# Kernel optimization log

Hardware: AMD Instinct MI355X
Metric: run time of the kernel (lower is better)

Reference implementation:

```python
import jax, jax.numpy as jnp
import numpy as np

AMPLITUDE_STD = 4.2  # repo constant (unexported); normalization scale for ln_mag
EPS = 1e-8


def _interp_bias(table, x):
    # Linear interpolation of a 1D table over frequency domain [-1, 1].
    n = table.shape[0]
    idx = jnp.clip((x + 1.0) * 0.5 * (n - 1), 0.0, float(n - 1))
    i0 = jnp.floor(idx).astype(jnp.int32)
    i1 = jnp.minimum(i0 + 1, n - 1)
    w = idx - i0.astype(idx.dtype)
    return table[i0] * (1.0 - w) + table[i1] * w


def setup_inputs() -> dict:
    key = jax.random.key(0)
    k1, k2, k3, k4 = jax.random.split(key, 4)
    B, F, P, W, H = 8, 128, 32, 96, 96
    return {
        "mode_shapes": jax.random.normal(k1, (B, 2, P, W, H), dtype=jnp.float32),
        "mode_responses": jax.random.normal(k2, (B, F, 2, P), dtype=jnp.float32),
        "freqs": jax.random.uniform(k3, (B, F), dtype=jnp.float32, minval=-1.0, maxval=1.0),
        "bias_table": jax.random.normal(k4, (250,), dtype=jnp.float32) * 0.1,
    }


def reference(mode_shapes, mode_responses, freqs, bias_table):
    B, _, P, W, H = mode_shapes.shape
    F = mode_responses.shape[1]
    # _normalize_mode: L2 norm over (real/imag, W, H) per (batch, peak)
    norm = jnp.sqrt(jnp.sum(mode_shapes ** 2, axis=(1, 3, 4)))  # (B,P)
    ms = mode_shapes / (norm[:, None, :, None, None] + EPS)
    s_r, s_i = ms[:, 0], ms[:, 1]                                # (B,P,W,H)
    t_r, t_i = mode_responses[:, :, 0], mode_responses[:, :, 1]  # (B,F,P)
    f = 1.0 / P
    # complex superposition over modes: contraction over n_peaks
    rr = jnp.einsum('bpwh,bfp->bfwh', s_r, t_r)
    ii = jnp.einsum('bpwh,bfp->bfwh', s_i, t_i)
    ri = jnp.einsum('bpwh,bfp->bfwh', s_r, t_i)
    ir = jnp.einsum('bpwh,bfp->bfwh', s_i, t_r)
    r_new = f * (rr - ii)  # (B,F,W,H)
    i_new = f * (ri + ir)
    mag2 = r_new ** 2 + i_new ** 2
    bias = _interp_bias(bias_table, freqs)                       # (B,F)
    ln_mag = (jnp.log(mag2 + EPS) + bias[:, :, None, None]) / AMPLITUDE_STD
    fnorm = jnp.sum(mag2, axis=(-1, -2), keepdims=True)
    fnorm = jnp.sqrt(jnp.clip(fnorm, jnp.finfo(fnorm.dtype).eps))
    normed_field = jnp.stack([r_new / fnorm, i_new / fnorm], axis=2)  # (B,F,2,W,H)
    # aux sparsity loss over mode responses
    mr = mode_responses.reshape(B, F * 2, P)
    aux_sparse = jnp.mean(jnp.mean(jnp.log(jnp.linalg.norm(mr, axis=1) + 1.0), axis=1))
    return ln_mag, normed_field, aux_sparse
```

## Files before the change

### kernel.cpp

```cpp
#include <hip/hip_runtime.h>
#include <math.h>

#define WHN 9216
#define PN 32
#define FN 128
#define BN 8
#define EPSF 1e-8f
#define INV_STD 0.23809523809f
#define AUX_IDX 28311552

typedef __attribute__((ext_vector_type(8))) short short8;
typedef __attribute__((ext_vector_type(16))) float f32x16;

__device__ __forceinline__ unsigned short f2bf(float x) {
  unsigned int u = __float_as_uint(x);
  unsigned int r = (u + 0x7FFFu + ((u >> 16) & 1u)) >> 16;
  return (unsigned short)r;
}
__device__ __forceinline__ float bf2f(unsigned short h) {
  return __uint_as_float(((unsigned int)h) << 16);
}

__global__ __launch_bounds__(256) void k_gram(const float* __restrict__ ms,
                                              float* __restrict__ wsM,
                                              float* __restrict__ wsA,
                                              float* __restrict__ part,
                                              int use_part) {
  const int b = blockIdx.y;
  const int chunk = blockIdx.x;
  const int tid = threadIdx.x;
  __shared__ float4 sA[32][32];
  __shared__ float4 sB[32][32];
  __shared__ float pbuf[2][2048];
  const float4* ms4 = (const float4*)ms;
#pragma unroll
  for (int k = 0; k < 4; ++k) {
    int i4 = tid + k * 256;
    int xq = i4 & 31, p = i4 >> 5;
    sA[xq][p ^ xq] = ms4[((b * 2 + 0) * 32 + p) * 2304 + chunk * 32 + xq];
    sB[xq][p ^ xq] = ms4[((b * 2 + 1) * 32 + p) * 2304 + chunk * 32 + xq];
  }
  __syncthreads();
  const int w = tid >> 6, lane = tid & 63;
  const int pg = lane & 7, qg = lane >> 3;
  float accM[4][4] = {{0}}, accA[4][4] = {{0}};
  for (int xq = w; xq < 32; xq += 4) {
    float4 pa[4], pb[4], qa[4], qb[4];
#pragma unroll
    for (int j = 0; j < 4; ++j) {
      pa[j] = sA[xq][(pg + 8 * j) ^ xq];
      pb[j] = sB[xq][(pg + 8 * j) ^ xq];
      qa[j] = sA[xq][(qg + 8 * j) ^ xq];
      qb[j] = sB[xq][(qg + 8 * j) ^ xq];
    }
#pragma unroll
    for (int j = 0; j < 4; ++j)
#pragma unroll
      for (int k = 0; k < 4; ++k) {
        accM[j][k] += pa[j].x * qa[k].x + pb[j].x * qb[k].x
                    + pa[j].y * qa[k].y + pb[j].y * qb[k].y
                    + pa[j].z * qa[k].z + pb[j].z * qb[k].z
                    + pa[j].w * qa[k].w + pb[j].w * qb[k].w;
        accA[j][k] += pa[j].x * qb[k].x - pb[j].x * qa[k].x
                    + pa[j].y * qb[k].y - pb[j].y * qa[k].y
                    + pa[j].z * qb[k].z - pb[j].z * qa[k].z
                    + pa[j].w * qb[k].w - pb[j].w * qa[k].w;
      }
  }
  if (w < 2) {
#pragma unroll
    for (int j = 0; j < 4; ++j)
#pragma unroll
      for (int k = 0; k < 4; ++k) {
        pbuf[w][lane * 32 + j * 4 + k] = accM[j][k];
        pbuf[w][lane * 32 + 16 + j * 4 + k] = accA[j][k];
      }
  }
  __syncthreads();
  if (w >= 2) {
#pragma unroll
    for (int j = 0; j < 4; ++j)
#pragma unroll
      for (int k = 0; k < 4; ++k) {
        pbuf[w - 2][lane * 32 + j * 4 + k] += accM[j][k];
        pbuf[w - 2][lane * 32 + 16 + j * 4 + k] += accA[j][k];
      }
  }
  __syncthreads();
  for (int idx = tid; idx < 2048; idx += 256) {
    float v = pbuf[0][idx] + pbuf[1][idx];
    if (use_part) {
      part[((size_t)(b * 72 + chunk)) * 2048 + idx] = v;
    } else {
      int lane2 = idx >> 5, r = idx & 31;
      int mat = r >> 4, rr = r & 15, j = rr >> 2, k = rr & 3;
      int p = (lane2 & 7) + 8 * j, q = (lane2 >> 3) + 8 * k;
      float* dst = mat ? wsA : wsM;
      atomicAdd(dst + (b << 10) + p * 32 + q, v);
    }
  }
}

__global__ __launch_bounds__(256) void k_reduce(const float* __restrict__ part,
                                                float* __restrict__ wsM,
                                                float* __restrict__ wsA,
                                                float* __restrict__ wsc) {
  int g = blockIdx.x * 256 + threadIdx.x;
  int b = g >> 11, idx = g & 2047;
  const float* p = part + ((size_t)b * 72) * 2048 + idx;
  float s = 0.f;
#pragma unroll 8
  for (int c = 0; c < 72; ++c) s += p[(size_t)c * 2048];
  int lane2 = idx >> 5, r = idx & 31;
  int mat = r >> 4, rr = r & 15, j = rr >> 2, k = rr & 3;
  int pp = (lane2 & 7) + 8 * j, q = (lane2 >> 3) + 8 * k;
  (mat ? wsA : wsM)[(b << 10) + pp * 32 + q] = s;
  if (!mat && pp == q) wsc[(b << 5) + pp] = (1.0f / 32.0f) / (sqrtf(s) + EPSF);
}

__global__ void k_cfromM(const float* __restrict__ wsM, float* __restrict__ wsc) {
  int tid = threadIdx.x;
  int b = tid >> 5, p = tid & 31;
  float m = wsM[(b << 10) + p * 33];
  wsc[tid] = (1.0f / 32.0f) / (sqrtf(m) + EPSF);
}

__global__ __launch_bounds__(256) void k_aux(const float* __restrict__ t,
                                             float* __restrict__ out) {
  const int b = blockIdx.x, tid = threadIdx.x;
  const float4* t4 = (const float4*)t + (size_t)b * 2048;
  float4 a; a.x = a.y = a.z = a.w = 0.f;
#pragma unroll
  for (int j = 0; j < 8; ++j) {
    float4 v = t4[tid + j * 256];
    a.x = fmaf(v.x, v.x, a.x);
    a.y = fmaf(v.y, v.y, a.y);
    a.z = fmaf(v.z, v.z, a.z);
    a.w = fmaf(v.w, v.w, a.w);
  }
#pragma unroll
  for (int off = 8; off <= 32; off <<= 1) {
    a.x += __shfl_xor(a.x, off);
    a.y += __shfl_xor(a.y, off);
    a.z += __shfl_xor(a.z, off);
    a.w += __shfl_xor(a.w, off);
  }
  __shared__ float sred[4][8][4];
  int wv = tid >> 6, lane = tid & 63;
  if (lane < 8) {
    sred[wv][lane][0] = a.x; sred[wv][lane][1] = a.y;
    sred[wv][lane][2] = a.z; sred[wv][lane][3] = a.w;
  }
  __syncthreads();
  if (tid < 8) {
    float s0 = 0, s1 = 0, s2 = 0, s3 = 0;
#pragma unroll
    for (int w2 = 0; w2 < 4; ++w2) {
      s0 += sred[w2][tid][0]; s1 += sred[w2][tid][1];
      s2 += sred[w2][tid][2]; s3 += sred[w2][tid][3];
    }
    float val = logf(sqrtf(s0) + 1.f) + logf(sqrtf(s1) + 1.f)
              + logf(sqrtf(s2) + 1.f) + logf(sqrtf(s3) + 1.f);
    val += __shfl_xor(val, 1);
    val += __shfl_xor(val, 2);
    val += __shfl_xor(val, 4);
    if (tid == 0) atomicAdd(out + AUX_IDX, val * (1.0f / 256.0f));
  }
}

__global__ __launch_bounds__(64) void k_fnorm(const float* __restrict__ t,
                                              const float* __restrict__ freqs,
                                              const float* __restrict__ btab,
                                              const float* __restrict__ wsM,
                                              const float* __restrict__ wsA,
                                              const float* __restrict__ wsc,
                                              float* __restrict__ wsinv,
                                              float* __restrict__ wsbias) {
  const int bf = blockIdx.x;
  const int b = bf >> 7;
  const int lane = threadIdx.x;
  __shared__ float tt[64];
  {
    int p = lane & 31, comp = lane >> 5;
    tt[lane] = t[(bf * 2 + comp) * PN + p] * wsc[(b << 5) + p];
  }
  __syncthreads();
  const int pp = lane & 31, qh = lane >> 5;
  const float* Mrow = wsM + (b << 10) + pp * 32 + qh * 16;
  const float* Arow = wsA + (b << 10) + pp * 32 + qh * 16;
  float ap = tt[pp], bp = tt[32 + pp];
  float S = 0.f;
#pragma unroll
  for (int k = 0; k < 16; ++k) {
    int q = qh * 16 + k;
    float aq = tt[q], bq = tt[32 + q];
    S += (ap * aq + bp * bq) * Mrow[k] + 2.0f * (bp * aq) * Arow[k];
  }
#pragma unroll
  for (int off = 32; off; off >>= 1) S += __shfl_xor(S, off);
  if (lane == 0) {
    float fn = sqrtf(fmaxf(S, 1.1920929e-7f));
    wsinv[bf] = 1.0f / fn;
    float x = freqs[bf];
    float idx = (x + 1.0f) * 0.5f * 249.0f;
    idx = fminf(fmaxf(idx, 0.0f), 249.0f);
    float fi = floorf(idx);
    int i0 = (int)fi;
    int i1 = min(i0 + 1, 249);
    float wvv = idx - fi;
    wsbias[bf] = btab[i0] * (1.0f - wvv) + btab[i1] * wvv;
  }
}

#define MFMA32(A, B, C) __builtin_amdgcn_mfma_f32_32x32x16_bf16(A, B, C, 0, 0, 0)
__global__ __launch_bounds__(256) void k_main(const float* __restrict__ ms,
                                              const float* __restrict__ t,
                                              const float* __restrict__ wsc,
                                              const float* __restrict__ wsinv,
                                              const float* __restrict__ wsbias,
                                              float* __restrict__ out) {
  __shared__ short tHs[8192];
  __shared__ short tLs[8192];
  __shared__ float sInv[128], sBias[128], sC[32];
  const int b = blockIdx.y;
  const int tid = threadIdx.x;
  const int lane = tid & 63, wv = tid >> 6;
  const int col = lane & 31, hf = lane >> 5;
  const int pix = blockIdx.x * 128 + wv * 32 + col;

  short8 sHf[4], sLf[4];
#pragma unroll
  for (int kg = 0; kg < 4; ++kg) {
#pragma unroll
    for (int j = 0; j < 8; ++j) {
      int k = kg * 16 + hf * 8 + j;
      float v = ms[(((size_t)b * 2 + (k >> 5)) * 32 + (k & 31)) * WHN + pix];
      unsigned short h = f2bf(v);
      sHf[kg][j] = (short)h;
      sLf[kg][j] = (short)f2bf(v - bf2f(h));
    }
  }
  short8 msk;
#pragma unroll
  for (int j = 0; j < 8; ++j) msk[j] = (short)0x8000;
  short8 nH2 = sHf[2] ^ msk, nL2 = sLf[2] ^ msk;
  short8 nH3 = sHf[3] ^ msk, nL3 = sLf[3] ^ msk;

  if (tid < 128) sInv[tid] = wsinv[b * 128 + tid];
  else sBias[tid - 128] = wsbias[b * 128 + (tid - 128)];
  if (tid < 32) sC[tid] = wsc[b * 32 + tid];
  __syncthreads();

#pragma unroll
  for (int it = 0; it < 4; ++it) {
    int gidx = tid + it * 256;
    int f = gidx >> 3, g = gidx & 7;
    const float* src = t + ((size_t)(b * 128 + f) * 2 + (g >> 2)) * 32 + (g & 3) * 8;
    int gs = g ^ (f & 7);
    short8 hv, lv;
#pragma unroll
    for (int e = 0; e < 8; ++e) {
      float v = src[e] * sC[(g & 3) * 8 + e];
      unsigned short h = f2bf(v);
      hv[e] = (short)h;
      lv[e] = (short)f2bf(v - bf2f(h));
    }
    *(short8*)&tHs[f * 64 + gs * 8] = hv;
    *(short8*)&tLs[f * 64 + gs * 8] = lv;
  }
  __syncthreads();

  float* outF = out + (size_t)BN * FN * WHN;

  for (int ft = 0; ft < 4; ++ft) {
    short8 tHf[4], tLf[4];
    int f = ft * 32 + col;
    int fx = f & 7;
#pragma unroll
    for (int kg = 0; kg < 4; ++kg) {
      int gs = (2 * kg + hf) ^ fx;
      tHf[kg] = *(const short8*)&tHs[f * 64 + gs * 8];
      tLf[kg] = *(const short8*)&tLs[f * 64 + gs * 8];
    }
    f32x16 aR, aI;
#pragma unroll
    for (int i = 0; i < 16; ++i) { aR[i] = 0.f; aI[i] = 0.f; }
    aR = MFMA32(tHf[0], sHf[0], aR); aR = MFMA32(tHf[0], sLf[0], aR); aR = MFMA32(tLf[0], sHf[0], aR);
    aR = MFMA32(tHf[1], sHf[1], aR); aR = MFMA32(tHf[1], sLf[1], aR); aR = MFMA32(tLf[1], sHf[1], aR);
    aR = MFMA32(tHf[2], nH2,    aR); aR = MFMA32(tHf[2], nL2,    aR); aR = MFMA32(tLf[2], nH2,    aR);
    aR = MFMA32(tHf[3], nH3,    aR); aR = MFMA32(tHf[3], nL3,    aR); aR = MFMA32(tLf[3], nH3,    aR);
    aI = MFMA32(tHf[0], sHf[2], aI); aI = MFMA32(tHf[0], sLf[2], aI); aI = MFMA32(tLf[0], sHf[2], aI);
    aI = MFMA32(tHf[1], sHf[3], aI); aI = MFMA32(tHf[1], sLf[3], aI); aI = MFMA32(tLf[1], sHf[3], aI);
    aI = MFMA32(tHf[2], sHf[0], aI); aI = MFMA32(tHf[2], sLf[0], aI); aI = MFMA32(tLf[2], sHf[0], aI);
    aI = MFMA32(tHf[3], sHf[1], aI); aI = MFMA32(tHf[3], sLf[1], aI); aI = MFMA32(tLf[3], sHf[1], aI);
#pragma unroll
    for (int r = 0; r < 16; ++r) {
      int row = (r & 3) + 8 * (r >> 2) + 4 * hf;
      int fo = ft * 32 + row;
      float vr = aR[r], vi = aI[r];
      float mag2 = fmaf(vr, vr, vi * vi);
      float ln = (__logf(mag2 + EPSF) + sBias[fo]) * INV_STD;
      float inv = sInv[fo];
      size_t fg = (size_t)(b * 128 + fo);
      out[fg * WHN + pix] = ln;
      outF[(fg * 2) * WHN + pix] = vr * inv;
      outF[(fg * 2 + 1) * WHN + pix] = vi * inv;
    }
  }
}

extern "C" void kernel_launch(void* const* d_in, const int* in_sizes, int n_in,
                              void* d_out, int out_size, void* d_ws, size_t ws_size,
                              hipStream_t stream) {
  const float* ms = (const float*)d_in[0];
  const float* t  = (const float*)d_in[1];
  const float* fr = (const float*)d_in[2];
  const float* bt = (const float*)d_in[3];
  float* out = (float*)d_out;
  float* ws = (float*)d_ws;
  float* wsM = ws;
  float* wsA = ws + 8192;
  float* wsc = ws + 16384;
  float* wsinv = ws + 16640;
  float* wsbias = ws + 17664;
  float* part = ws + 18688;
  size_t need = ((size_t)18688 + (size_t)576 * 2048) * 4;
  int use_part = (ws_size >= need) ? 1 : 0;

  hipMemsetAsync((char*)d_out + (size_t)AUX_IDX * 4, 0, 4, stream);
  if (use_part) {
    hipLaunchKernelGGL(k_gram, dim3(72, 8), dim3(256), 0, stream, ms, wsM, wsA, part, 1);
    hipLaunchKernelGGL(k_reduce, dim3(64), dim3(256), 0, stream, part, wsM, wsA, wsc);
  } else {
    hipMemsetAsync(ws, 0, 16384 * sizeof(float), stream);
    hipLaunchKernelGGL(k_gram, dim3(72, 8), dim3(256), 0, stream, ms, wsM, wsA, part, 0);
    hipLaunchKernelGGL(k_cfromM, dim3(1), dim3(256), 0, stream, wsM, wsc);
  }
  hipLaunchKernelGGL(k_fnorm, dim3(1024), dim3(64), 0, stream, t, fr, bt, wsM, wsA, wsc, wsinv, wsbias);
  hipLaunchKernelGGL(k_aux, dim3(8), dim3(256), 0, stream, t, out);
  hipLaunchKernelGGL(k_main, dim3(72, 8), dim3(256), 0, stream, ms, t, wsc, wsinv, wsbias, out);
}
```

Measured before the change: 168.9 us.

## Split main kernel over frequency halves, fold aux into fnorm, drop memset

```diff
diff --git a/kernel.cpp b/kernel.cpp
--- a/kernel.cpp
+++ b/kernel.cpp
@@ -101,11 +101,13 @@
   }
 }
 
-__global__ __launch_bounds__(256) void k_reduce(const float* __restrict__ part,
-                                                float* __restrict__ wsM,
-                                                float* __restrict__ wsA,
-                                                float* __restrict__ wsc) {
+__global__ __launch_bounds__(256) void k_mid(const float* __restrict__ part,
+                                             float* __restrict__ wsM,
+                                             float* __restrict__ wsA,
+                                             float* __restrict__ wsc,
+                                             float* __restrict__ out) {
   int g = blockIdx.x * 256 + threadIdx.x;
+  if (g == 0) out[AUX_IDX] = 0.f;
   int b = g >> 11, idx = g & 2047;
   const float* p = part + ((size_t)b * 72) * 2048 + idx;
   float s = 0.f;
@@ -118,67 +120,43 @@
   if (!mat && pp == q) wsc[(b << 5) + pp] = (1.0f / 32.0f) / (sqrtf(s) + EPSF);
 }
 
-__global__ void k_cfromM(const float* __restrict__ wsM, float* __restrict__ wsc) {
+__global__ void k_cfromM(const float* __restrict__ wsM, float* __restrict__ wsc,
+                         float* __restrict__ out) {
   int tid = threadIdx.x;
+  if (tid == 0) out[AUX_IDX] = 0.f;
   int b = tid >> 5, p = tid & 31;
   float m = wsM[(b << 10) + p * 33];
   wsc[tid] = (1.0f / 32.0f) / (sqrtf(m) + EPSF);
 }
 
-__global__ __launch_bounds__(256) void k_aux(const float* __restrict__ t,
-                                             float* __restrict__ out) {
-  const int b = blockIdx.x, tid = threadIdx.x;
-  const float4* t4 = (const float4*)t + (size_t)b * 2048;
-  float4 a; a.x = a.y = a.z = a.w = 0.f;
-#pragma unroll
-  for (int j = 0; j < 8; ++j) {
-    float4 v = t4[tid + j * 256];
-    a.x = fmaf(v.x, v.x, a.x);
-    a.y = fmaf(v.y, v.y, a.y);
-    a.z = fmaf(v.z, v.z, a.z);
-    a.w = fmaf(v.w, v.w, a.w);
-  }
-#pragma unroll
-  for (int off = 8; off <= 32; off <<= 1) {
-    a.x += __shfl_xor(a.x, off);
-    a.y += __shfl_xor(a.y, off);
-    a.z += __shfl_xor(a.z, off);
-    a.w += __shfl_xor(a.w, off);
-  }
-  __shared__ float sred[4][8][4];
-  int wv = tid >> 6, lane = tid & 63;
-  if (lane < 8) {
-    sred[wv][lane][0] = a.x; sred[wv][lane][1] = a.y;
-    sred[wv][lane][2] = a.z; sred[wv][lane][3] = a.w;
-  }
-  __syncthreads();
-  if (tid < 8) {
-    float s0 = 0, s1 = 0, s2 = 0, s3 = 0;
-#pragma unroll
-    for (int w2 = 0; w2 < 4; ++w2) {
-      s0 += sred[w2][tid][0]; s1 += sred[w2][tid][1];
-      s2 += sred[w2][tid][2]; s3 += sred[w2][tid][3];
-    }
-    float val = logf(sqrtf(s0) + 1.f) + logf(sqrtf(s1) + 1.f)
-              + logf(sqrtf(s2) + 1.f) + logf(sqrtf(s3) + 1.f);
-    val += __shfl_xor(val, 1);
-    val += __shfl_xor(val, 2);
-    val += __shfl_xor(val, 4);
-    if (tid == 0) atomicAdd(out + AUX_IDX, val * (1.0f / 256.0f));
-  }
-}
-
-__global__ __launch_bounds__(64) void k_fnorm(const float* __restrict__ t,
-                                              const float* __restrict__ freqs,
-                                              const float* __restrict__ btab,
-                                              const float* __restrict__ wsM,
-                                              const float* __restrict__ wsA,
-                                              const float* __restrict__ wsc,
-                                              float* __restrict__ wsinv,
-                                              float* __restrict__ wsbias) {
+__global__ __launch_bounds__(64) void k_fnb(const float* __restrict__ t,
+                                            const float* __restrict__ freqs,
+                                            const float* __restrict__ btab,
+                                            const float* __restrict__ wsM,
+                                            const float* __restrict__ wsA,
+                                            const float* __restrict__ wsc,
+                                            float* __restrict__ wsinv,
+                                            float* __restrict__ wsbias,
+                                            float* __restrict__ out) {
+  const int lane = threadIdx.x;
+  if (blockIdx.x >= 1024) {
+    const int b = blockIdx.x - 1024;
+    const int p = lane & 31, comp = lane >> 5;
+    float acc = 0.f;
+#pragma unroll 4
+    for (int f = 0; f < FN; ++f) {
+      float v = t[((size_t)(b * FN + f) * 2 + comp) * PN + p];
+      acc = fmaf(v, v, acc);
+    }
+    acc += __shfl_xor(acc, 32);
+    float val = logf(sqrtf(acc) + 1.0f);
+#pragma unroll
+    for (int off = 1; off <= 16; off <<= 1) val += __shfl_xor(val, off);
+    if (lane == 0) atomicAdd(out + AUX_IDX, val * (1.0f / 256.0f));
+    return;
+  }
   const int bf = blockIdx.x;
   const int b = bf >> 7;
-  const int lane = threadIdx.x;
   __shared__ float tt[64];
   {
     int p = lane & 31, comp = lane >> 5;
@@ -219,22 +197,24 @@
                                               const float* __restrict__ wsinv,
                                               const float* __restrict__ wsbias,
                                               float* __restrict__ out) {
-  __shared__ short tHs[8192];
-  __shared__ short tLs[8192];
-  __shared__ float sInv[128], sBias[128], sC[32];
+  __shared__ short tHs[4096];
+  __shared__ short tLs[4096];
+  __shared__ float sInv[64], sBias[64], sC[32];
   const int b = blockIdx.y;
   const int tid = threadIdx.x;
   const int lane = tid & 63, wv = tid >> 6;
   const int col = lane & 31, hf = lane >> 5;
   const int pix = blockIdx.x * 128 + wv * 32 + col;
-
+  const int f0 = blockIdx.z * 64;
+
+  const float* msb = ms + (size_t)b * 64 * WHN + pix;
   short8 sHf[4], sLf[4];
 #pragma unroll
   for (int kg = 0; kg < 4; ++kg) {
 #pragma unroll
     for (int j = 0; j < 8; ++j) {
       int k = kg * 16 + hf * 8 + j;
-      float v = ms[(((size_t)b * 2 + (k >> 5)) * 32 + (k & 31)) * WHN + pix];
+      float v = msb[(size_t)k * WHN];
       unsigned short h = f2bf(v);
       sHf[kg][j] = (short)h;
       sLf[kg][j] = (short)f2bf(v - bf2f(h));
@@ -246,17 +226,17 @@
   short8 nH2 = sHf[2] ^ msk, nL2 = sLf[2] ^ msk;
   short8 nH3 = sHf[3] ^ msk, nL3 = sLf[3] ^ msk;
 
-  if (tid < 128) sInv[tid] = wsinv[b * 128 + tid];
-  else sBias[tid - 128] = wsbias[b * 128 + (tid - 128)];
-  if (tid < 32) sC[tid] = wsc[b * 32 + tid];
-  __syncthreads();
-
-#pragma unroll
-  for (int it = 0; it < 4; ++it) {
+  if (tid < 64) sInv[tid] = wsinv[b * 128 + f0 + tid];
+  else if (tid < 128) sBias[tid - 64] = wsbias[b * 128 + f0 + (tid - 64)];
+  if (tid >= 224) sC[tid - 224] = wsc[b * 32 + (tid - 224)];
+  __syncthreads();
+
+#pragma unroll
+  for (int it = 0; it < 2; ++it) {
     int gidx = tid + it * 256;
-    int f = gidx >> 3, g = gidx & 7;
-    const float* src = t + ((size_t)(b * 128 + f) * 2 + (g >> 2)) * 32 + (g & 3) * 8;
-    int gs = g ^ (f & 7);
+    int fl = gidx >> 3, g = gidx & 7;
+    const float* src = t + ((size_t)(b * 128 + f0 + fl) * 2 + (g >> 2)) * 32 + (g & 3) * 8;
+    int gs = g ^ (fl & 7);
     short8 hv, lv;
 #pragma unroll
     for (int e = 0; e < 8; ++e) {
@@ -265,22 +245,23 @@
       hv[e] = (short)h;
       lv[e] = (short)f2bf(v - bf2f(h));
     }
-    *(short8*)&tHs[f * 64 + gs * 8] = hv;
-    *(short8*)&tLs[f * 64 + gs * 8] = lv;
+    *(short8*)&tHs[fl * 64 + gs * 8] = hv;
+    *(short8*)&tLs[fl * 64 + gs * 8] = lv;
   }
   __syncthreads();
 
   float* outF = out + (size_t)BN * FN * WHN;
 
-  for (int ft = 0; ft < 4; ++ft) {
+#pragma unroll
+  for (int ft = 0; ft < 2; ++ft) {
     short8 tHf[4], tLf[4];
-    int f = ft * 32 + col;
-    int fx = f & 7;
+    int fl = ft * 32 + col;
+    int fx = fl & 7;
 #pragma unroll
     for (int kg = 0; kg < 4; ++kg) {
       int gs = (2 * kg + hf) ^ fx;
-      tHf[kg] = *(const short8*)&tHs[f * 64 + gs * 8];
-      tLf[kg] = *(const short8*)&tLs[f * 64 + gs * 8];
+      tHf[kg] = *(const short8*)&tHs[fl * 64 + gs * 8];
+      tLf[kg] = *(const short8*)&tLs[fl * 64 + gs * 8];
     }
     f32x16 aR, aI;
 #pragma unroll
@@ -301,10 +282,10 @@
       float mag2 = fmaf(vr, vr, vi * vi);
       float ln = (__logf(mag2 + EPSF) + sBias[fo]) * INV_STD;
       float inv = sInv[fo];
-      size_t fg = (size_t)(b * 128 + fo);
-      out[fg * WHN + pix] = ln;
-      outF[(fg * 2) * WHN + pix] = vr * inv;
-      outF[(fg * 2 + 1) * WHN + pix] = vi * inv;
+      size_t fg = (size_t)(b * 128 + f0 + fo);
+      __builtin_nontemporal_store(ln, out + fg * WHN + pix);
+      __builtin_nontemporal_store(vr * inv, outF + (fg * 2) * WHN + pix);
+      __builtin_nontemporal_store(vi * inv, outF + (fg * 2 + 1) * WHN + pix);
     }
   }
 }
@@ -327,16 +308,14 @@
   size_t need = ((size_t)18688 + (size_t)576 * 2048) * 4;
   int use_part = (ws_size >= need) ? 1 : 0;
 
-  hipMemsetAsync((char*)d_out + (size_t)AUX_IDX * 4, 0, 4, stream);
   if (use_part) {
     hipLaunchKernelGGL(k_gram, dim3(72, 8), dim3(256), 0, stream, ms, wsM, wsA, part, 1);
-    hipLaunchKernelGGL(k_reduce, dim3(64), dim3(256), 0, stream, part, wsM, wsA, wsc);
+    hipLaunchKernelGGL(k_mid, dim3(64), dim3(256), 0, stream, part, wsM, wsA, wsc, out);
   } else {
     hipMemsetAsync(ws, 0, 16384 * sizeof(float), stream);
     hipLaunchKernelGGL(k_gram, dim3(72, 8), dim3(256), 0, stream, ms, wsM, wsA, part, 0);
-    hipLaunchKernelGGL(k_cfromM, dim3(1), dim3(256), 0, stream, wsM, wsc);
-  }
-  hipLaunchKernelGGL(k_fnorm, dim3(1024), dim3(64), 0, stream, t, fr, bt, wsM, wsA, wsc, wsinv, wsbias);
-  hipLaunchKernelGGL(k_aux, dim3(8), dim3(256), 0, stream, t, out);
-  hipLaunchKernelGGL(k_main, dim3(72, 8), dim3(256), 0, stream, ms, t, wsc, wsinv, wsbias, out);
-}
+    hipLaunchKernelGGL(k_cfromM, dim3(1), dim3(256), 0, stream, wsM, wsc, out);
+  }
+  hipLaunchKernelGGL(k_fnb, dim3(1032), dim3(64), 0, stream, t, fr, bt, wsM, wsA, wsc, wsinv, wsbias, out);
+  hipLaunchKernelGGL(k_main, dim3(72, 8, 2), dim3(256), 0, stream, ms, t, wsc, wsinv, wsbias, out);
+}
```

New measurement: 171.6 us. No clear change (+1.6%).
